# Performance work log

Hardware: AMD Instinct MI355X
Metric: run time of the kernel (lower is better)

Reference implementation:

```python
import jax, jax.numpy as jnp
import numpy as np

N_ENT = 40000
N_REL = 500
N = N_ENT + N_REL
EMB = 256
N_EDGES = 648000
BATCH = 1024
BN_EPS = 1e-5


def make_hamilton(kernel):
    # kernel: [in//4, out]; returns [in, out] quaternion (Hamilton) weight
    r, i, j, k = jnp.split(kernel, 4, axis=1)
    r2 = jnp.concatenate([r, -i, -j, -k], axis=0)
    i2 = jnp.concatenate([i, r, -k, j], axis=0)
    j2 = jnp.concatenate([j, k, r, -i], axis=0)
    k2 = jnp.concatenate([k, -j, i, r], axis=0)
    return jnp.concatenate([r2, i2, j2, k2], axis=1)


def setup_inputs() -> dict:
    key = jax.random.key(0)
    ks = jax.random.split(key, 8)
    e1_idx = jax.random.randint(ks[0], (BATCH,), 0, N_ENT, dtype=jnp.int32)
    r_idx = jax.random.randint(ks[1], (BATCH,), 0, N_REL, dtype=jnp.int32)
    lst_indexes = jnp.arange(N, dtype=jnp.int32)
    emb_weight = jax.random.normal(ks[2], (N, EMB), dtype=jnp.float32) * 0.05
    qgnn_weight = jax.random.normal(ks[3], (EMB // 4, EMB), dtype=jnp.float32) * 0.1
    edge_src = jax.random.randint(ks[4], (N_EDGES,), 0, N, dtype=jnp.int32)
    edge_dst = jax.random.randint(ks[5], (N_EDGES,), 0, N, dtype=jnp.int32)
    edge_val = jax.random.uniform(ks[6], (N_EDGES,), dtype=jnp.float32)
    bn_gamma = jnp.ones((EMB,), dtype=jnp.float32)
    bn_beta = jnp.zeros((EMB,), dtype=jnp.float32)
    return {"e1_idx": e1_idx, "r_idx": r_idx, "lst_indexes": lst_indexes,
            "emb_weight": emb_weight, "qgnn_weight": qgnn_weight,
            "edge_src": edge_src, "edge_dst": edge_dst, "edge_val": edge_val,
            "bn_gamma": bn_gamma, "bn_beta": bn_beta}


def reference(e1_idx, r_idx, lst_indexes, emb_weight, qgnn_weight,
              edge_src, edge_dst, edge_val, bn_gamma, bn_beta):
    # Embedding lookup over all nodes (entities + relations)
    X = emb_weight[lst_indexes]                       # [N, EMB]
    # QGNN layer: Hamilton-product transform, sparse adj aggregation, tanh
    hamilton = make_hamilton(qgnn_weight)             # [EMB, EMB]
    support = X @ hamilton                            # [N, EMB]
    msgs = edge_val[:, None] * support[edge_dst]      # [E, EMB]
    agg = jax.ops.segment_sum(msgs, edge_src, num_segments=N)
    X = jnp.tanh(agg)                                 # [N, EMB]
    # DistMult scoring
    h = X[e1_idx]                                     # [B, EMB]
    r = X[r_idx + N_ENT]                              # [B, EMB]
    hr = h * r
    # BatchNorm1d (training-mode batch statistics, biased variance)
    mean = jnp.mean(hr, axis=0)
    var = jnp.var(hr, axis=0)
    hr = (hr - mean) * jax.lax.rsqrt(var + BN_EPS) * bn_gamma + bn_beta
    # Dropout is identity in deterministic/eval reference
    hrt = hr @ X[:N_ENT].T                            # [B, N_ENT]
    return jax.nn.sigmoid(hrt)
```

## Files before the change

kernel.cpp:

```cpp
#include <hip/hip_runtime.h>
#include <math.h>

#define N_ENT 40000
#define N_NODES 40500
#define EMB 256
#define N_EDGES 648000
#define BATCH 1024
#define BN_EPS 1e-5f
#define SCAN_NB 40

typedef __attribute__((ext_vector_type(8))) _Float16 half8;
typedef __attribute__((ext_vector_type(4))) _Float16 half4v;
typedef __attribute__((ext_vector_type(4))) float f32x4;

__device__ __forceinline__ void gl_lds16(const void* g, void* l) {
    __builtin_amdgcn_global_load_lds(
        (const __attribute__((address_space(1))) void*)g,
        (__attribute__((address_space(3))) void*)l, 16, 0, 0);
}

__global__ void build_hamilton_h(const float* __restrict__ qw,
                                 _Float16* __restrict__ Hth) {
    int idx = blockIdx.x * 256 + threadIdx.x;
    int o = idx >> 8, i = idx & 255;
    int p = i >> 6, i0 = i & 63;
    int q = o >> 6, o0 = o & 63;
    const int   ctab[16] = {0,1,2,3, 1,0,3,2, 2,3,0,1, 3,2,1,0};
    const float stab[16] = {1.f,1.f,1.f,1.f, -1.f,1.f,1.f,-1.f, -1.f,-1.f,1.f,1.f, -1.f,1.f,-1.f,1.f};
    float v = stab[p*4+q] * qw[i0*EMB + ctab[p*4+q]*64 + o0];
    Hth[idx] = (_Float16)v;
}

__global__ __launch_bounds__(256) void support_mfma(const float* __restrict__ emb,
                                                    const _Float16* __restrict__ Hth,
                                                    _Float16* __restrict__ Ch) {
    const int wid  = threadIdx.x >> 6;
    const int lane = threadIdx.x & 63;
    const int wr = wid >> 1, wc = wid & 1;
    const int row0 = blockIdx.x * 64 + wr * 32;
    const int col0 = wc * 128;
    const int fr = lane & 15;
    const int kg = lane >> 4;
    f32x4 acc[2][8] = {};
    for (int kb = 0; kb < 8; ++kb) {
        const int koff = kb * 32 + kg * 8;
        half8 a[2];
        #pragma unroll
        for (int i = 0; i < 2; ++i) {
            int r = row0 + i * 16 + fr;
            if (r > N_NODES - 1) r = N_NODES - 1;
            const float* src = emb + (size_t)r * EMB + koff;
            float4 va = *(const float4*)(src);
            float4 vb = *(const float4*)(src + 4);
            a[i][0] = (_Float16)va.x; a[i][1] = (_Float16)va.y;
            a[i][2] = (_Float16)va.z; a[i][3] = (_Float16)va.w;
            a[i][4] = (_Float16)vb.x; a[i][5] = (_Float16)vb.y;
            a[i][6] = (_Float16)vb.z; a[i][7] = (_Float16)vb.w;
        }
        half8 b[8];
        #pragma unroll
        for (int j = 0; j < 8; ++j)
            b[j] = *(const half8*)(Hth + (size_t)(col0 + j * 16 + fr) * EMB + koff);
        #pragma unroll
        for (int i = 0; i < 2; ++i)
            #pragma unroll
            for (int j = 0; j < 8; ++j)
                acc[i][j] = __builtin_amdgcn_mfma_f32_16x16x32_f16(a[i], b[j], acc[i][j], 0, 0, 0);
    }
    #pragma unroll
    for (int i = 0; i < 2; ++i) {
        int rbase = row0 + i * 16 + (lane >> 4) * 4;
        #pragma unroll
        for (int j = 0; j < 8; ++j) {
            int c = col0 + j * 16 + (lane & 15);
            #pragma unroll
            for (int r = 0; r < 4; ++r) {
                if (rbase + r < N_NODES)
                    Ch[(size_t)(rbase + r) * EMB + c] = (_Float16)acc[i][j][r];
            }
        }
    }
}

__global__ void hist_k(const int* __restrict__ src, int* __restrict__ cnt) {
    int e = blockIdx.x * 256 + threadIdx.x;
    if (e < N_EDGES) atomicAdd(&cnt[src[e]], 1);
}

__global__ __launch_bounds__(1024) void scan_blocks(const int* __restrict__ cnt,
                                                    int* __restrict__ row_start,
                                                    int* __restrict__ bsum) {
    __shared__ int wsum[16];
    const int t = threadIdx.x;
    const int lane = t & 63, wid = t >> 6;
    int idx = blockIdx.x * 1024 + t;
    int v = (idx < N_NODES) ? cnt[idx] : 0;
    int incl = v;
    #pragma unroll
    for (int off = 1; off < 64; off <<= 1) {
        int u = __shfl_up(incl, off);
        if (lane >= off) incl += u;
    }
    if (lane == 63) wsum[wid] = incl;
    __syncthreads();
    if (t < 16) {
        int wv = wsum[t];
        #pragma unroll
        for (int off = 1; off < 16; off <<= 1) {
            int u = __shfl_up(wv, off);
            if (t >= off) wv += u;
        }
        wsum[t] = wv;
    }
    __syncthreads();
    int woff = (wid > 0) ? wsum[wid - 1] : 0;
    incl += woff;
    if (idx < N_NODES) row_start[idx] = incl - v;
    if (t == 1023) bsum[blockIdx.x] = incl;
}

__global__ void scan_tops(int* __restrict__ bsum) {
    int t = threadIdx.x;
    int v = (t < SCAN_NB) ? bsum[t] : 0;
    int incl = v;
    #pragma unroll
    for (int off = 1; off < 64; off <<= 1) {
        int u = __shfl_up(incl, off);
        if (t >= off) incl += u;
    }
    if (t < SCAN_NB) bsum[t] = incl - v;
    if (t == SCAN_NB - 1) bsum[SCAN_NB] = incl;
}

__global__ __launch_bounds__(1024) void scan_add(int* __restrict__ row_start,
                                                 int* __restrict__ cursor,
                                                 const int* __restrict__ bsum) {
    int idx = blockIdx.x * 1024 + threadIdx.x;
    if (idx < N_NODES) {
        int v = row_start[idx] + bsum[blockIdx.x];
        row_start[idx] = v;
        cursor[idx] = v;
    }
    if (idx == N_NODES) row_start[N_NODES] = bsum[SCAN_NB];
}

__global__ void place_edges(const int* __restrict__ src, const int* __restrict__ dst,
                            const float* __restrict__ val, int* __restrict__ cursor,
                            int* __restrict__ dst_s, float* __restrict__ val_s) {
    int e = blockIdx.x * 256 + threadIdx.x;
    if (e >= N_EDGES) return;
    int pos = atomicAdd(&cursor[src[e]], 1);
    dst_s[pos] = dst[e];
    val_s[pos] = val[e];
}

__global__ __launch_bounds__(256) void spmm_tanh(const int* __restrict__ row_start,
                                                 const int* __restrict__ dst_s,
                                                 const float* __restrict__ val_s,
                                                 const _Float16* __restrict__ support_h,
                                                 _Float16* __restrict__ Xh) {
    int row = blockIdx.x * 4 + (threadIdx.x >> 6);
    if (row >= N_NODES) return;
    int lane = threadIdx.x & 63;
    int beg = row_start[row], end = row_start[row + 1];
    float4 acc = make_float4(0.f, 0.f, 0.f, 0.f);
    for (int i = beg; i < end; ++i) {
        int d = dst_s[i];
        float v = val_s[i];
        half4v x = *(const half4v*)(support_h + (size_t)d * EMB + lane * 4);
        acc.x = fmaf(v, (float)x[0], acc.x);
        acc.y = fmaf(v, (float)x[1], acc.y);
        acc.z = fmaf(v, (float)x[2], acc.z);
        acc.w = fmaf(v, (float)x[3], acc.w);
    }
    half4v o;
    o[0] = (_Float16)tanhf(acc.x); o[1] = (_Float16)tanhf(acc.y);
    o[2] = (_Float16)tanhf(acc.z); o[3] = (_Float16)tanhf(acc.w);
    *(half4v*)(Xh + (size_t)row * EMB + lane * 4) = o;
}

__global__ void hr_k(const _Float16* __restrict__ Xh, const int* __restrict__ e1,
                     const int* __restrict__ ri, float* __restrict__ hr) {
    int b = blockIdx.x, f = threadIdx.x;
    float h = (float)Xh[(size_t)e1[b] * EMB + f];
    float r = (float)Xh[((size_t)ri[b] + N_ENT) * EMB + f];
    hr[b * EMB + f] = h * r;
}

__global__ __launch_bounds__(256) void bn_stats(const float* __restrict__ hr,
                                                float* __restrict__ mean,
                                                float* __restrict__ var) {
    int f = blockIdx.x, t = threadIdx.x;
    float s = 0.f, sq = 0.f;
    for (int b = t; b < BATCH; b += 256) {
        float v = hr[b * EMB + f];
        s += v; sq += v * v;
    }
    #pragma unroll
    for (int off = 32; off > 0; off >>= 1) {
        s  += __shfl_down(s, off);
        sq += __shfl_down(sq, off);
    }
    __shared__ float ss[4], sqs[4];
    int w = t >> 6;
    if ((t & 63) == 0) { ss[w] = s; sqs[w] = sq; }
    __syncthreads();
    if (t == 0) {
        s  = ss[0] + ss[1] + ss[2] + ss[3];
        sq = sqs[0] + sqs[1] + sqs[2] + sqs[3];
        float m = s * (1.f / BATCH);
        mean[f] = m;
        var[f] = sq * (1.f / BATCH) - m * m;
    }
}

__global__ void bn_apply_h(const float* __restrict__ hr, const float* __restrict__ mean,
                           const float* __restrict__ var, const float* __restrict__ gamma,
                           const float* __restrict__ beta, _Float16* __restrict__ hr_h) {
    int idx = blockIdx.x * 256 + threadIdx.x;
    int f = idx & 255;
    float inv = rsqrtf(var[f] + BN_EPS);
    float v = (hr[idx] - mean[f]) * inv * gamma[f] + beta[f];
    hr_h[idx] = (_Float16)v;
}

__global__ __launch_bounds__(256) void score_v3(const _Float16* __restrict__ hr_h,
                                                const _Float16* __restrict__ Xh,
                                                float* __restrict__ out) {
    __shared__ char smem[64 * 132 * 4];
    _Float16* As = (_Float16*)smem;
    _Float16* Bs = As + 2048;
    float* Ep = (float*)smem;

    const int tid  = threadIdx.x;
    const int wid  = tid >> 6;
    const int lane = tid & 63;
    const int wr = wid >> 1, wc = wid & 1;
    const int row0 = blockIdx.x * 64;
    const int col0 = blockIdx.y * 128;
    const int fr = lane & 15;
    const int kg = lane >> 4;
    const int lrow = lane >> 2;
    const int lchk = (lane & 3) * 8;

    f32x4 acc[2][4] = {};

    for (int kb = 0; kb < 8; ++kb) {
        const int koff = kb * 32;
        #pragma unroll
        for (int c = 0; c < 3; ++c) {
            int ch = wid * 3 + c;
            if (ch < 4) {
                int lr = ch * 16 + lrow;
                const _Float16* srcA = hr_h + (size_t)(row0 + lr) * EMB + koff + lchk;
                gl_lds16(srcA, smem + ch * 1024);
            } else {
                int br = (ch - 4) * 16 + lrow;
                int gc = col0 + br;
                if (gc > N_ENT - 1) gc = N_ENT - 1;
                const _Float16* srcB = Xh + (size_t)gc * EMB + koff + lchk;
                gl_lds16(srcB, smem + ch * 1024);
            }
        }
        __syncthreads();
        half8 a_[2], b_[4];
        #pragma unroll
        for (int i = 0; i < 2; ++i) {
            int r = wr * 32 + i * 16 + fr;
            a_[i] = *(const half8*)&As[r * 32 + kg * 8];
        }
        #pragma unroll
        for (int j = 0; j < 4; ++j) {
            int r = wc * 64 + j * 16 + fr;
            b_[j] = *(const half8*)&Bs[r * 32 + kg * 8];
        }
        #pragma unroll
        for (int i = 0; i < 2; ++i)
            #pragma unroll
            for (int j = 0; j < 4; ++j)
                acc[i][j] = __builtin_amdgcn_mfma_f32_16x16x32_f16(a_[i], b_[j], acc[i][j], 0, 0, 0);
        __syncthreads();
    }

    #pragma unroll
    for (int i = 0; i < 2; ++i) {
        int rl = wr * 32 + i * 16 + (lane >> 4) * 4;
        #pragma unroll
        for (int j = 0; j < 4; ++j) {
            int cl = wc * 64 + j * 16 + (lane & 15);
            #pragma unroll
            for (int r = 0; r < 4; ++r)
                Ep[(rl + r) * 132 + cl] = 1.f / (1.f + __expf(-acc[i][j][r]));
        }
    }
    __syncthreads();
    #pragma unroll
    for (int it = 0; it < 8; ++it) {
        int idx = it * 256 + tid;
        int row = idx >> 5;
        int c4 = (idx & 31) << 2;
        f32x4 v = *(const f32x4*)&Ep[row * 132 + c4];
        int gc = col0 + c4;
        if (gc < N_ENT)
            __builtin_nontemporal_store(v, (f32x4*)(out + (size_t)(row0 + row) * N_ENT + gc));
    }
}

extern "C" void kernel_launch(void* const* d_in, const int* in_sizes, int n_in,
                              void* d_out, int out_size, void* d_ws, size_t ws_size,
                              hipStream_t stream) {
    const int*   e1    = (const int*)d_in[0];
    const int*   ri    = (const int*)d_in[1];
    const float* emb   = (const float*)d_in[3];
    const float* qw    = (const float*)d_in[4];
    const int*   esrc  = (const int*)d_in[5];
    const int*   edst  = (const int*)d_in[6];
    const float* evalv = (const float*)d_in[7];
    const float* gamma = (const float*)d_in[8];
    const float* beta  = (const float*)d_in[9];
    float* out = (float*)d_out;

    const size_t NODE_F = (size_t)N_NODES * EMB;
    _Float16* support_h = (_Float16*)d_ws;
    _Float16* Xh        = support_h + NODE_F;
    float*    hr        = (float*)(Xh + NODE_F);
    float*    mean      = hr + 262144;
    float*    var       = mean + 256;
    int*      row_start = (int*)(var + 256);
    int*      cnt       = row_start + (N_NODES + 1);
    int*      cursor    = cnt + N_NODES;
    int*      bsum      = cursor + N_NODES;
    int*      dst_s     = bsum + SCAN_NB + 1;
    float*    val_s     = (float*)(dst_s + N_EDGES);
    _Float16* hr_h      = (_Float16*)(val_s + N_EDGES);
    _Float16* Hth       = hr_h + 262144;

    hipMemsetAsync(cnt, 0, N_NODES * sizeof(int), stream);
    hist_k<<<(N_EDGES + 255) / 256, 256, 0, stream>>>(esrc, cnt);
    scan_blocks<<<SCAN_NB, 1024, 0, stream>>>(cnt, row_start, bsum);
    scan_tops<<<1, 64, 0, stream>>>(bsum);
    scan_add<<<SCAN_NB, 1024, 0, stream>>>(row_start, cursor, bsum);

    build_hamilton_h<<<256, 256, 0, stream>>>(qw, Hth);
    support_mfma<<<633, 256, 0, stream>>>(emb, Hth, support_h);

    place_edges<<<(N_EDGES + 255) / 256, 256, 0, stream>>>(esrc, edst, evalv, cursor, dst_s, val_s);
    spmm_tanh<<<N_NODES / 4, 256, 0, stream>>>(row_start, dst_s, val_s, support_h, Xh);

    hr_k<<<BATCH, 256, 0, stream>>>(Xh, e1, ri, hr);
    bn_stats<<<EMB, 256, 0, stream>>>(hr, mean, var);
    bn_apply_h<<<1024, 256, 0, stream>>>(hr, mean, var, gamma, beta, hr_h);
    score_v3<<<dim3(16, 313), 256, 0, stream>>>(hr_h, Xh, out);
}
```

Baseline: 279.0 us.

## Fuse small kernels, pack CSR edges, and unroll SpMM gather loop

Merges the scan-blocks pass with Hamilton weight construction, folds the top-level scan into scan_add, and runs the support GEMM and edge placement as two block ranges of a single launch. Edge destination and value are packed into one int2 array, and the SpMM loop is unrolled by four so that several gathers are in flight at once. The hr product, BN statistics and BN apply are fused into one kernel so the fp32 hr buffer is never written out. This cuts launch count and intermediate traffic, but the fused BN kernel reads the feature column with a stride across rows, which gives uncoalesced gathers.

```diff
diff --git a/kernel.cpp b/kernel.cpp
--- a/kernel.cpp
+++ b/kernel.cpp
@@ -19,21 +19,98 @@
         (__attribute__((address_space(3))) void*)l, 16, 0, 0);
 }
 
-__global__ void build_hamilton_h(const float* __restrict__ qw,
-                                 _Float16* __restrict__ Hth) {
-    int idx = blockIdx.x * 256 + threadIdx.x;
-    int o = idx >> 8, i = idx & 255;
-    int p = i >> 6, i0 = i & 63;
-    int q = o >> 6, o0 = o & 63;
-    const int   ctab[16] = {0,1,2,3, 1,0,3,2, 2,3,0,1, 3,2,1,0};
-    const float stab[16] = {1.f,1.f,1.f,1.f, -1.f,1.f,1.f,-1.f, -1.f,-1.f,1.f,1.f, -1.f,1.f,-1.f,1.f};
-    float v = stab[p*4+q] * qw[i0*EMB + ctab[p*4+q]*64 + o0];
-    Hth[idx] = (_Float16)v;
-}
-
-__global__ __launch_bounds__(256) void support_mfma(const float* __restrict__ emb,
-                                                    const _Float16* __restrict__ Hth,
-                                                    _Float16* __restrict__ Ch) {
+__global__ void hist_k(const int* __restrict__ src, int* __restrict__ cnt) {
+    int e = blockIdx.x * 256 + threadIdx.x;
+    if (e < N_EDGES) atomicAdd(&cnt[src[e]], 1);
+}
+
+__global__ __launch_bounds__(1024) void scanham(const int* __restrict__ cnt,
+                                                int* __restrict__ row_start,
+                                                int* __restrict__ bsum,
+                                                const float* __restrict__ qw,
+                                                _Float16* __restrict__ Hth) {
+    const int t = threadIdx.x;
+    if (blockIdx.x < SCAN_NB) {
+        __shared__ int wsum[16];
+        const int lane = t & 63, wid = t >> 6;
+        int idx = blockIdx.x * 1024 + t;
+        int v = (idx < N_NODES) ? cnt[idx] : 0;
+        int incl = v;
+        #pragma unroll
+        for (int off = 1; off < 64; off <<= 1) {
+            int u = __shfl_up(incl, off);
+            if (lane >= off) incl += u;
+        }
+        if (lane == 63) wsum[wid] = incl;
+        __syncthreads();
+        if (t < 16) {
+            int wv = wsum[t];
+            #pragma unroll
+            for (int off = 1; off < 16; off <<= 1) {
+                int u = __shfl_up(wv, off);
+                if (t >= off) wv += u;
+            }
+            wsum[t] = wv;
+        }
+        __syncthreads();
+        int woff = (wid > 0) ? wsum[wid - 1] : 0;
+        incl += woff;
+        if (idx < N_NODES) row_start[idx] = incl - v;
+        if (t == 1023) bsum[blockIdx.x] = incl;
+    } else {
+        int idx = (blockIdx.x - SCAN_NB) * 1024 + t;
+        int o = idx >> 8, i = idx & 255;
+        int p = i >> 6, i0 = i & 63;
+        int q = o >> 6, o0 = o & 63;
+        const int   ctab[16] = {0,1,2,3, 1,0,3,2, 2,3,0,1, 3,2,1,0};
+        const float stab[16] = {1.f,1.f,1.f,1.f, -1.f,1.f,1.f,-1.f, -1.f,-1.f,1.f,1.f, -1.f,1.f,-1.f,1.f};
+        Hth[idx] = (_Float16)(stab[p*4+q] * qw[i0*EMB + ctab[p*4+q]*64 + o0]);
+    }
+}
+
+__global__ __launch_bounds__(1024) void scan_add(int* __restrict__ row_start,
+                                                 int* __restrict__ cursor,
+                                                 const int* __restrict__ bsum) {
+    __shared__ int off_s, tot_s;
+    const int t = threadIdx.x;
+    if (t < 64) {
+        int v = (t < SCAN_NB) ? bsum[t] : 0;
+        int incl = v;
+        #pragma unroll
+        for (int off = 1; off < 64; off <<= 1) {
+            int u = __shfl_up(incl, off);
+            if (t >= off) incl += u;
+        }
+        int off = (blockIdx.x == 0) ? 0 : __shfl(incl, (int)blockIdx.x - 1);
+        int tot = __shfl(incl, SCAN_NB - 1);
+        if (t == 0) { off_s = off; tot_s = tot; }
+    }
+    __syncthreads();
+    int idx = blockIdx.x * 1024 + t;
+    if (idx < N_NODES) {
+        int v = row_start[idx] + off_s;
+        row_start[idx] = v;
+        cursor[idx] = v;
+    }
+    if (idx == N_NODES) row_start[N_NODES] = tot_s;
+}
+
+__global__ __launch_bounds__(256) void support_place(const float* __restrict__ emb,
+                                                     const _Float16* __restrict__ Hth,
+                                                     _Float16* __restrict__ Ch,
+                                                     const int* __restrict__ esrc,
+                                                     const int* __restrict__ edst,
+                                                     const float* __restrict__ evalv,
+                                                     int* __restrict__ cursor,
+                                                     int2* __restrict__ edge_s) {
+    if (blockIdx.x >= 633) {
+        int e = (blockIdx.x - 633) * 256 + threadIdx.x;
+        if (e < N_EDGES) {
+            int pos = atomicAdd(&cursor[esrc[e]], 1);
+            edge_s[pos] = make_int2(edst[e], __float_as_int(evalv[e]));
+        }
+        return;
+    }
     const int wid  = threadIdx.x >> 6;
     const int lane = threadIdx.x & 63;
     const int wr = wid >> 1, wc = wid & 1;
@@ -82,81 +159,8 @@
     }
 }
 
-__global__ void hist_k(const int* __restrict__ src, int* __restrict__ cnt) {
-    int e = blockIdx.x * 256 + threadIdx.x;
-    if (e < N_EDGES) atomicAdd(&cnt[src[e]], 1);
-}
-
-__global__ __launch_bounds__(1024) void scan_blocks(const int* __restrict__ cnt,
-                                                    int* __restrict__ row_start,
-                                                    int* __restrict__ bsum) {
-    __shared__ int wsum[16];
-    const int t = threadIdx.x;
-    const int lane = t & 63, wid = t >> 6;
-    int idx = blockIdx.x * 1024 + t;
-    int v = (idx < N_NODES) ? cnt[idx] : 0;
-    int incl = v;
-    #pragma unroll
-    for (int off = 1; off < 64; off <<= 1) {
-        int u = __shfl_up(incl, off);
-        if (lane >= off) incl += u;
-    }
-    if (lane == 63) wsum[wid] = incl;
-    __syncthreads();
-    if (t < 16) {
-        int wv = wsum[t];
-        #pragma unroll
-        for (int off = 1; off < 16; off <<= 1) {
-            int u = __shfl_up(wv, off);
-            if (t >= off) wv += u;
-        }
-        wsum[t] = wv;
-    }
-    __syncthreads();
-    int woff = (wid > 0) ? wsum[wid - 1] : 0;
-    incl += woff;
-    if (idx < N_NODES) row_start[idx] = incl - v;
-    if (t == 1023) bsum[blockIdx.x] = incl;
-}
-
-__global__ void scan_tops(int* __restrict__ bsum) {
-    int t = threadIdx.x;
-    int v = (t < SCAN_NB) ? bsum[t] : 0;
-    int incl = v;
-    #pragma unroll
-    for (int off = 1; off < 64; off <<= 1) {
-        int u = __shfl_up(incl, off);
-        if (t >= off) incl += u;
-    }
-    if (t < SCAN_NB) bsum[t] = incl - v;
-    if (t == SCAN_NB - 1) bsum[SCAN_NB] = incl;
-}
-
-__global__ __launch_bounds__(1024) void scan_add(int* __restrict__ row_start,
-                                                 int* __restrict__ cursor,
-                                                 const int* __restrict__ bsum) {
-    int idx = blockIdx.x * 1024 + threadIdx.x;
-    if (idx < N_NODES) {
-        int v = row_start[idx] + bsum[blockIdx.x];
-        row_start[idx] = v;
-        cursor[idx] = v;
-    }
-    if (idx == N_NODES) row_start[N_NODES] = bsum[SCAN_NB];
-}
-
-__global__ void place_edges(const int* __restrict__ src, const int* __restrict__ dst,
-                            const float* __restrict__ val, int* __restrict__ cursor,
-                            int* __restrict__ dst_s, float* __restrict__ val_s) {
-    int e = blockIdx.x * 256 + threadIdx.x;
-    if (e >= N_EDGES) return;
-    int pos = atomicAdd(&cursor[src[e]], 1);
-    dst_s[pos] = dst[e];
-    val_s[pos] = val[e];
-}
-
 __global__ __launch_bounds__(256) void spmm_tanh(const int* __restrict__ row_start,
-                                                 const int* __restrict__ dst_s,
-                                                 const float* __restrict__ val_s,
+                                                 const int2* __restrict__ edge_s,
                                                  const _Float16* __restrict__ support_h,
                                                  _Float16* __restrict__ Xh) {
     int row = blockIdx.x * 4 + (threadIdx.x >> 6);
@@ -164,10 +168,28 @@
     int lane = threadIdx.x & 63;
     int beg = row_start[row], end = row_start[row + 1];
     float4 acc = make_float4(0.f, 0.f, 0.f, 0.f);
-    for (int i = beg; i < end; ++i) {
-        int d = dst_s[i];
-        float v = val_s[i];
-        half4v x = *(const half4v*)(support_h + (size_t)d * EMB + lane * 4);
+    int i = beg;
+    for (; i + 3 < end; i += 4) {
+        int2 e0 = edge_s[i], e1 = edge_s[i+1], e2 = edge_s[i+2], e3 = edge_s[i+3];
+        half4v x0 = *(const half4v*)(support_h + (size_t)e0.x * EMB + lane * 4);
+        half4v x1 = *(const half4v*)(support_h + (size_t)e1.x * EMB + lane * 4);
+        half4v x2 = *(const half4v*)(support_h + (size_t)e2.x * EMB + lane * 4);
+        half4v x3 = *(const half4v*)(support_h + (size_t)e3.x * EMB + lane * 4);
+        float v0 = __int_as_float(e0.y), v1 = __int_as_float(e1.y);
+        float v2 = __int_as_float(e2.y), v3 = __int_as_float(e3.y);
+        acc.x = fmaf(v0, (float)x0[0], acc.x); acc.y = fmaf(v0, (float)x0[1], acc.y);
+        acc.z = fmaf(v0, (float)x0[2], acc.z); acc.w = fmaf(v0, (float)x0[3], acc.w);
+        acc.x = fmaf(v1, (float)x1[0], acc.x); acc.y = fmaf(v1, (float)x1[1], acc.y);
+        acc.z = fmaf(v1, (float)x1[2], acc.z); acc.w = fmaf(v1, (float)x1[3], acc.w);
+        acc.x = fmaf(v2, (float)x2[0], acc.x); acc.y = fmaf(v2, (float)x2[1], acc.y);
+        acc.z = fmaf(v2, (float)x2[2], acc.z); acc.w = fmaf(v2, (float)x2[3], acc.w);
+        acc.x = fmaf(v3, (float)x3[0], acc.x); acc.y = fmaf(v3, (float)x3[1], acc.y);
+        acc.z = fmaf(v3, (float)x3[2], acc.z); acc.w = fmaf(v3, (float)x3[3], acc.w);
+    }
+    for (; i < end; ++i) {
+        int2 e = edge_s[i];
+        float v = __int_as_float(e.y);
+        half4v x = *(const half4v*)(support_h + (size_t)e.x * EMB + lane * 4);
         acc.x = fmaf(v, (float)x[0], acc.x);
         acc.y = fmaf(v, (float)x[1], acc.y);
         acc.z = fmaf(v, (float)x[2], acc.z);
@@ -179,29 +201,29 @@
     *(half4v*)(Xh + (size_t)row * EMB + lane * 4) = o;
 }
 
-__global__ void hr_k(const _Float16* __restrict__ Xh, const int* __restrict__ e1,
-                     const int* __restrict__ ri, float* __restrict__ hr) {
-    int b = blockIdx.x, f = threadIdx.x;
-    float h = (float)Xh[(size_t)e1[b] * EMB + f];
-    float r = (float)Xh[((size_t)ri[b] + N_ENT) * EMB + f];
-    hr[b * EMB + f] = h * r;
-}
-
-__global__ __launch_bounds__(256) void bn_stats(const float* __restrict__ hr,
-                                                float* __restrict__ mean,
-                                                float* __restrict__ var) {
-    int f = blockIdx.x, t = threadIdx.x;
+__global__ __launch_bounds__(256) void bn_fused(const _Float16* __restrict__ Xh,
+                                                const int* __restrict__ e1,
+                                                const int* __restrict__ ri,
+                                                const float* __restrict__ gamma,
+                                                const float* __restrict__ beta,
+                                                _Float16* __restrict__ hr_h) {
+    const int f = blockIdx.x, t = threadIdx.x;
+    float v[4];
     float s = 0.f, sq = 0.f;
-    for (int b = t; b < BATCH; b += 256) {
-        float v = hr[b * EMB + f];
-        s += v; sq += v * v;
+    #pragma unroll
+    for (int k = 0; k < 4; ++k) {
+        int b = t + k * 256;
+        float h = (float)Xh[(size_t)e1[b] * EMB + f];
+        float r = (float)Xh[((size_t)ri[b] + N_ENT) * EMB + f];
+        v[k] = h * r;
+        s += v[k]; sq += v[k] * v[k];
     }
     #pragma unroll
     for (int off = 32; off > 0; off >>= 1) {
         s  += __shfl_down(s, off);
         sq += __shfl_down(sq, off);
     }
-    __shared__ float ss[4], sqs[4];
+    __shared__ float ss[4], sqs[4], mv[2];
     int w = t >> 6;
     if ((t & 63) == 0) { ss[w] = s; sqs[w] = sq; }
     __syncthreads();
@@ -209,19 +231,18 @@
         s  = ss[0] + ss[1] + ss[2] + ss[3];
         sq = sqs[0] + sqs[1] + sqs[2] + sqs[3];
         float m = s * (1.f / BATCH);
-        mean[f] = m;
-        var[f] = sq * (1.f / BATCH) - m * m;
-    }
-}
-
-__global__ void bn_apply_h(const float* __restrict__ hr, const float* __restrict__ mean,
-                           const float* __restrict__ var, const float* __restrict__ gamma,
-                           const float* __restrict__ beta, _Float16* __restrict__ hr_h) {
-    int idx = blockIdx.x * 256 + threadIdx.x;
-    int f = idx & 255;
-    float inv = rsqrtf(var[f] + BN_EPS);
-    float v = (hr[idx] - mean[f]) * inv * gamma[f] + beta[f];
-    hr_h[idx] = (_Float16)v;
+        mv[0] = m;
+        mv[1] = sq * (1.f / BATCH) - m * m;
+    }
+    __syncthreads();
+    float mean = mv[0];
+    float inv = rsqrtf(mv[1] + BN_EPS) * gamma[f];
+    float bet = beta[f];
+    #pragma unroll
+    for (int k = 0; k < 4; ++k) {
+        int b = t + k * 256;
+        hr_h[(size_t)b * EMB + f] = (_Float16)((v[k] - mean) * inv + bet);
+    }
 }
 
 __global__ __launch_bounds__(256) void score_v3(const _Float16* __restrict__ hr_h,
@@ -323,32 +344,21 @@
     const size_t NODE_F = (size_t)N_NODES * EMB;
     _Float16* support_h = (_Float16*)d_ws;
     _Float16* Xh        = support_h + NODE_F;
-    float*    hr        = (float*)(Xh + NODE_F);
-    float*    mean      = hr + 262144;
-    float*    var       = mean + 256;
-    int*      row_start = (int*)(var + 256);
+    int*      row_start = (int*)(Xh + NODE_F);
     int*      cnt       = row_start + (N_NODES + 1);
     int*      cursor    = cnt + N_NODES;
     int*      bsum      = cursor + N_NODES;
-    int*      dst_s     = bsum + SCAN_NB + 1;
-    float*    val_s     = (float*)(dst_s + N_EDGES);
-    _Float16* hr_h      = (_Float16*)(val_s + N_EDGES);
+    int2*     edge_s    = (int2*)(bsum + SCAN_NB + 1);
+    _Float16* hr_h      = (_Float16*)(edge_s + N_EDGES);
     _Float16* Hth       = hr_h + 262144;
 
     hipMemsetAsync(cnt, 0, N_NODES * sizeof(int), stream);
     hist_k<<<(N_EDGES + 255) / 256, 256, 0, stream>>>(esrc, cnt);
-    scan_blocks<<<SCAN_NB, 1024, 0, stream>>>(cnt, row_start, bsum);
-    scan_tops<<<1, 64, 0, stream>>>(bsum);
+    scanham<<<SCAN_NB + 64, 1024, 0, stream>>>(cnt, row_start, bsum, qw, Hth);
     scan_add<<<SCAN_NB, 1024, 0, stream>>>(row_start, cursor, bsum);
-
-    build_hamilton_h<<<256, 256, 0, stream>>>(qw, Hth);
-    support_mfma<<<633, 256, 0, stream>>>(emb, Hth, support_h);
-
-    place_edges<<<(N_EDGES + 255) / 256, 256, 0, stream>>>(esrc, edst, evalv, cursor, dst_s, val_s);
-    spmm_tanh<<<N_NODES / 4, 256, 0, stream>>>(row_start, dst_s, val_s, support_h, Xh);
-
-    hr_k<<<BATCH, 256, 0, stream>>>(Xh, e1, ri, hr);
-    bn_stats<<<EMB, 256, 0, stream>>>(hr, mean, var);
-    bn_apply_h<<<1024, 256, 0, stream>>>(hr, mean, var, gamma, beta, hr_h);
+    support_place<<<633 + (N_EDGES + 255) / 256, 256, 0, stream>>>(
+        emb, Hth, support_h, esrc, edst, evalv, cursor, edge_s);
+    spmm_tanh<<<N_NODES / 4, 256, 0, stream>>>(row_start, edge_s, support_h, Xh);
+    bn_fused<<<EMB, 256, 0, stream>>>(Xh, e1, ri, gamma, beta, hr_h);
     score_v3<<<dim3(16, 313), 256, 0, stream>>>(hr_h, Xh, out);
 }
```

Result: faster. 226.0 us (-19.0%).
